# Kernel optimization log

Hardware: AMD Instinct MI355X
Metric: run time of the kernel (lower is better)

The kernel has to match this reference:

```python
import jax, jax.numpy as jnp
import numpy as np


def setup_inputs() -> dict:
    key = jax.random.key(0)
    k1, k2, k3, k4 = jax.random.split(key, 4)
    B, S, E, D = 8, 2048, 1024, 64
    return {
        "sequence": jax.random.normal(k1, (B, S, E), dtype=jnp.float32),
        "Wk": jax.random.normal(k2, (E, D), dtype=jnp.float32) * (E ** -0.5),
        "Wq": jax.random.normal(k3, (E, D), dtype=jnp.float32) * (E ** -0.5),
        "Wv": jax.random.normal(k4, (E, D), dtype=jnp.float32) * (E ** -0.5),
    }


def reference(sequence, Wk, Wq, Wv):
    # sequence: [B, S, E]; Wk/Wq/Wv: [E, D]
    B, S, E = sequence.shape
    D = Wk.shape[-1]
    k = sequence @ Wk  # [B, S, D]
    q = sequence @ Wq  # [B, S, D]
    v = sequence @ Wv  # [B, S, D]
    scores = jnp.einsum("bqd,bkd->bqk", q, k) * (D ** -0.5)  # [B, S, S]
    causal = jnp.tril(jnp.ones((S, S), dtype=bool))
    scores = jnp.where(causal, scores, -jnp.inf)
    attn = jax.nn.softmax(scores, axis=-1)  # [B, S, S]
    out = jnp.einsum("bqk,bkd->bqd", attn, v)  # [B, S, D]
    return (out, attn)
```

## Files before the change

kernel.cpp:

```cpp
#include <hip/hip_runtime.h>
#include <hip/hip_bf16.h>


typedef __attribute__((ext_vector_type(8))) __bf16 bf16x8;
typedef __attribute__((ext_vector_type(4))) float f32x4;

constexpr int S_LEN = 2048;

__device__ inline unsigned short f2bf(float f) {
  union { float f; unsigned u; } v; v.f = f;
  unsigned u = v.u + 0x7FFFu + ((v.u >> 16) & 1u);
  return (unsigned short)(u >> 16);
}
__device__ inline float bf2f(unsigned short s) {
  union { unsigned u; float f; } v; v.u = ((unsigned)s) << 16;
  return v.f;
}

__device__ inline uint4 pack8u(float4 f0, float4 f1) {
  union { __hip_bfloat162 h[4]; uint4 v; } u;
  u.h[0] = __float22bfloat162_rn(float2{f0.x, f0.y});
  u.h[1] = __float22bfloat162_rn(float2{f0.z, f0.w});
  u.h[2] = __float22bfloat162_rn(float2{f1.x, f1.y});
  u.h[3] = __float22bfloat162_rn(float2{f1.z, f1.w});
  return u.v;
}

__global__ __launch_bounds__(256) void wt_conv(
    const float* __restrict__ Wq, const float* __restrict__ Wk,
    const float* __restrict__ Wv, unsigned short* __restrict__ wt) {
  __shared__ float T[64][65];
  const int mat = blockIdx.y;
  const int k0 = blockIdx.x * 64;
  const float* W = (mat == 0) ? Wq : ((mat == 1) ? Wk : Wv);
  const int t = threadIdx.x;

  for (int s = 0; s < 4; ++s) {
    int rr = (t >> 4) + s * 16;
    int cc = (t & 15) * 4;
    float4 f = *(const float4*)(W + (size_t)(k0 + rr) * 64 + cc);
    T[rr][cc] = f.x; T[rr][cc + 1] = f.y; T[rr][cc + 2] = f.z; T[rr][cc + 3] = f.w;
  }
  __syncthreads();
  const float sc = (mat == 0) ? 0.125f : 1.0f;
  const int n = t >> 2, kc = (t & 3) * 16;
  union { unsigned short s[16]; uint4 v[2]; } tmp;
  for (int i = 0; i < 16; ++i) tmp.s[i] = f2bf(T[kc + i][n] * sc);
  unsigned short* dst = wt + (size_t)(mat * 64 + n) * 1024 + k0 + kc;
  *(uint4*)dst = tmp.v[0];
  *(uint4*)(dst + 8) = tmp.v[1];
}

__global__ __launch_bounds__(256) void qkv_gemm(
    const float* __restrict__ seq, const unsigned short* __restrict__ wt,
    unsigned short* __restrict__ qb, unsigned short* __restrict__ kb,
    unsigned short* __restrict__ vt) {
  __shared__ unsigned short As[2][32][72];
  const int row0 = blockIdx.x * 32;
  const int t = threadIdx.x;
  const int wv = t >> 6, lane = t & 63, lm = lane & 15, lq = lane >> 4;

  f32x4 acc[6];
  for (int i = 0; i < 6; ++i) acc[i] = (f32x4){0.f, 0.f, 0.f, 0.f};

  const int srow = t >> 3, skc = (t & 7) * 8;
  const float* ap = seq + (size_t)(row0 + srow) * 1024 + skc;

  float4 f0 = *(const float4*)ap;
  float4 f1 = *(const float4*)(ap + 4);
  *(uint4*)&As[0][srow][skc] = pack8u(f0, f1);

  for (int i = 0; i < 16; ++i) {
    if (i < 15) {
      f0 = *(const float4*)(ap + (i + 1) * 64);
      f1 = *(const float4*)(ap + (i + 1) * 64 + 4);
    }
    __syncthreads();
    const int buf = i & 1;
    for (int ks = 0; ks < 2; ++ks) {
      bf16x8 a0 = *(const bf16x8*)&As[buf][lm][ks * 32 + lq * 8];
      bf16x8 a1 = *(const bf16x8*)&As[buf][16 + lm][ks * 32 + lq * 8];
      for (int nt = 0; nt < 3; ++nt) {
        const unsigned short* bp =
            wt + (size_t)(wv * 48 + nt * 16 + lm) * 1024 + i * 64 + ks * 32 + lq * 8;
        bf16x8 bfr = *(const bf16x8*)bp;
        acc[nt] = __builtin_amdgcn_mfma_f32_16x16x32_bf16(a0, bfr, acc[nt], 0, 0, 0);
        acc[3 + nt] = __builtin_amdgcn_mfma_f32_16x16x32_bf16(a1, bfr, acc[3 + nt], 0, 0, 0);
      }
    }
    if (i < 15) *(uint4*)&As[buf ^ 1][srow][skc] = pack8u(f0, f1);
  }

  const int bb = row0 >> 11;
  const int s0 = row0 & (S_LEN - 1);
  for (int nt = 0; nt < 3; ++nt) {
    int ng = wv * 48 + nt * 16 + lm;
    int mat = ng >> 6, d = ng & 63;
    for (int mt = 0; mt < 2; ++mt) {
      f32x4 v = acc[mt * 3 + nt];
      if (mat == 2) {
        ushort4 u;
        u.x = f2bf(v[0]); u.y = f2bf(v[1]); u.z = f2bf(v[2]); u.w = f2bf(v[3]);
        *(ushort4*)(vt + ((size_t)(bb * 64 + d)) * S_LEN + s0 + mt * 16 + lq * 4) = u;
      } else {
        unsigned short* dst = mat ? kb : qb;
        for (int r = 0; r < 4; ++r)
          dst[(size_t)(row0 + mt * 16 + lq * 4 + r) * 64 + d] = f2bf(v[r]);
      }
    }
  }
}

__global__ __launch_bounds__(256) void attn_stats(
    const unsigned short* __restrict__ qb, const unsigned short* __restrict__ kb,
    float* __restrict__ lbuf) {
  __shared__ unsigned short Ks[128][72];
  const int q0 = blockIdx.x * 64, c0 = blockIdx.y * 512, b = blockIdx.z;
  if (c0 >= q0 + 64) return;
  const int kend = min(c0 + 512, q0 + 64);
  const int t = threadIdx.x, wv = t >> 6, lane = t & 63, lm = lane & 15, lq = lane >> 4;

  const unsigned short* qp = qb + ((size_t)(b * S_LEN + q0 + wv * 16 + lm)) * 64 + lq * 8;
  bf16x8 qf0 = *(const bf16x8*)qp;
  bf16x8 qf1 = *(const bf16x8*)(qp + 32);
  const int rw0 = q0 + wv * 16;

  float lp[4] = {0.f, 0.f, 0.f, 0.f};
  const int sr = t >> 3, sc = (t & 7) * 8;

  for (int kk = c0; kk < kend; kk += 128) {
    __syncthreads();
    const unsigned short* src = kb + ((size_t)(b * S_LEN + kk)) * 64;
    for (int j = 0; j < 4; ++j)
      *(uint4*)&Ks[j * 32 + sr][sc] = *(const uint4*)(src + (size_t)(j * 32 + sr) * 64 + sc);
    __syncthreads();
    if (kk <= rw0 + 15) {
      int ktmax = min(8, (rw0 + 15 - kk) / 16 + 1);
      for (int kt = 0; kt < ktmax; ++kt) {
        int key = kk + kt * 16 + lm;
        f32x4 z = (f32x4){0.f, 0.f, 0.f, 0.f};
        bf16x8 k0 = *(const bf16x8*)&Ks[kt * 16 + lm][lq * 8];
        bf16x8 k1 = *(const bf16x8*)&Ks[kt * 16 + lm][32 + lq * 8];
        z = __builtin_amdgcn_mfma_f32_16x16x32_bf16(qf0, k0, z, 0, 0, 0);
        z = __builtin_amdgcn_mfma_f32_16x16x32_bf16(qf1, k1, z, 0, 0, 0);
        for (int r = 0; r < 4; ++r) {
          float e = __expf(z[r]);
          lp[r] += (key <= rw0 + lq * 4 + r) ? e : 0.f;
        }
      }
    }
  }
  for (int off = 1; off < 16; off <<= 1)
    for (int r = 0; r < 4; ++r) lp[r] += __shfl_xor(lp[r], off);
  if (lm == 0)
    for (int r = 0; r < 4; ++r)
      unsafeAtomicAdd(&lbuf[b * S_LEN + rw0 + lq * 4 + r], lp[r]);
}

__global__ __launch_bounds__(256) void attn_write(
    const unsigned short* __restrict__ qb, const unsigned short* __restrict__ kb,
    const unsigned short* __restrict__ vt, const float* __restrict__ lbuf,
    float* __restrict__ outp, float* __restrict__ attnp) {
  __shared__ unsigned short Ks[256][72];
  __shared__ unsigned short Ps[4][16][72];
  const int q0 = blockIdx.x * 64, c0 = blockIdx.y * 256, b = blockIdx.z;
  const int t = threadIdx.x, wv = t >> 6, lane = t & 63, lm = lane & 15, lq = lane >> 4;
  float* arow = attnp + (size_t)b * S_LEN * S_LEN;

  if (c0 >= q0 + 64) {
    const int col = (t & 63) * 4, r0 = t >> 6;
    float4 z4 = {0.f, 0.f, 0.f, 0.f};
    for (int rr = r0; rr < 64; rr += 4)
      *(float4*)(arow + (size_t)(q0 + rr) * S_LEN + c0 + col) = z4;
    return;
  }

  {
    const int sr = t >> 3, sc = (t & 7) * 8;
    const unsigned short* src = kb + ((size_t)(b * S_LEN + c0)) * 64;
    for (int j = 0; j < 8; ++j)
      *(uint4*)&Ks[j * 32 + sr][sc] = *(const uint4*)(src + (size_t)(j * 32 + sr) * 64 + sc);
  }
  const unsigned short* qp = qb + ((size_t)(b * S_LEN + q0 + wv * 16 + lm)) * 64 + lq * 8;
  bf16x8 qf0 = *(const bf16x8*)qp;
  bf16x8 qf1 = *(const bf16x8*)(qp + 32);
  const int rw0 = q0 + wv * 16;

  float il[4];
  for (int r = 0; r < 4; ++r) il[r] = 1.0f / lbuf[b * S_LEN + rw0 + lq * 4 + r];

  f32x4 o[4];
  for (int i = 0; i < 4; ++i) o[i] = (f32x4){0.f, 0.f, 0.f, 0.f};
  __syncthreads();

  for (int st = 0; st < 4; ++st) {
    const int kk0 = c0 + st * 64;
    if (kk0 > rw0 + 15) {
      float4 z4 = {0.f, 0.f, 0.f, 0.f};
      for (int r4 = 0; r4 < 4; ++r4)
        *(float4*)(arow + (size_t)(rw0 + r4 * 4 + lq) * S_LEN + kk0 + lm * 4) = z4;
      continue;
    }
    f32x4 c4[4];
    for (int kt = 0; kt < 4; ++kt) {
      f32x4 z = (f32x4){0.f, 0.f, 0.f, 0.f};
      bf16x8 k0 = *(const bf16x8*)&Ks[st * 64 + kt * 16 + lm][lq * 8];
      bf16x8 k1 = *(const bf16x8*)&Ks[st * 64 + kt * 16 + lm][32 + lq * 8];
      z = __builtin_amdgcn_mfma_f32_16x16x32_bf16(qf0, k0, z, 0, 0, 0);
      z = __builtin_amdgcn_mfma_f32_16x16x32_bf16(qf1, k1, z, 0, 0, 0);
      c4[kt] = z;
    }
    bf16x8 vf[2][4];
    for (int ks2 = 0; ks2 < 2; ++ks2)
      for (int nt = 0; nt < 4; ++nt)
        vf[ks2][nt] = *(const bf16x8*)(vt + ((size_t)(b * 64 + nt * 16 + lm)) * S_LEN +
                                       kk0 + ks2 * 32 + lq * 8);
    for (int kt = 0; kt < 4; ++kt) {
      int key = kk0 + kt * 16 + lm;
      for (int r = 0; r < 4; ++r) {
        int rw = rw0 + lq * 4 + r;
        float p = (key > rw) ? 0.f : __expf(c4[kt][r]) * il[r];
        Ps[wv][lq * 4 + r][kt * 16 + lm] = f2bf(p);
      }
    }
    for (int ks2 = 0; ks2 < 2; ++ks2) {
      bf16x8 pa = *(const bf16x8*)&Ps[wv][lm][ks2 * 32 + lq * 8];
      for (int nt = 0; nt < 4; ++nt)
        o[nt] = __builtin_amdgcn_mfma_f32_16x16x32_bf16(pa, vf[ks2][nt], o[nt], 0, 0, 0);
    }
    for (int r4 = 0; r4 < 4; ++r4) {
      int row2 = r4 * 4 + lq;
      ushort4 u = *(const ushort4*)&Ps[wv][row2][lm * 4];
      float4 f;
      f.x = bf2f(u.x); f.y = bf2f(u.y); f.z = bf2f(u.z); f.w = bf2f(u.w);
      *(float4*)(arow + (size_t)(rw0 + row2) * S_LEN + kk0 + lm * 4) = f;
    }
  }

  for (int nt = 0; nt < 4; ++nt)
    for (int r = 0; r < 4; ++r)
      unsafeAtomicAdd(outp + ((size_t)(b * S_LEN + rw0 + lq * 4 + r)) * 64 + nt * 16 + lm,
                      o[nt][r]);
}

extern "C" void kernel_launch(void* const* d_in, const int* in_sizes, int n_in,
                              void* d_out, int out_size, void* d_ws, size_t ws_size,
                              hipStream_t stream) {
  const float* seq = (const float*)d_in[0];
  const float* Wk  = (const float*)d_in[1];
  const float* Wq  = (const float*)d_in[2];
  const float* Wv  = (const float*)d_in[3];

  float* outp = (float*)d_out;
  float* attnp = outp + (size_t)8 * S_LEN * 64;

  unsigned short* qb = (unsigned short*)d_ws;
  unsigned short* kb = qb + (size_t)16384 * 64;
  unsigned short* vt = kb + (size_t)16384 * 64;
  unsigned short* wt = vt + (size_t)8 * 64 * S_LEN;
  float* lbuf = (float*)(wt + (size_t)192 * 1024);

  hipMemsetAsync(lbuf, 0, (size_t)16384 * 4, stream);
  hipMemsetAsync(outp, 0, (size_t)8 * S_LEN * 64 * 4, stream);

  wt_conv<<<dim3(16, 3), 256, 0, stream>>>(Wq, Wk, Wv, wt);
  qkv_gemm<<<dim3(512, 1), 256, 0, stream>>>(seq, wt, qb, kb, vt);
  attn_stats<<<dim3(32, 4, 8), 256, 0, stream>>>(qb, kb, lbuf);
  attn_write<<<dim3(32, 8, 8), 256, 0, stream>>>(qb, kb, vt, lbuf, outp, attnp);
}
```

Before: 250.9 us.

## Stage weights in LDS for QKV GEMM, drop K LDS staging, use nontemporal attn stores

The QKV GEMM now runs with 512 threads and double-buffers both the activation tile and the full 192-column weight tile in shared memory, so B fragments are no longer fetched from global memory by every wave. The attention stats and write kernels drop their shared-memory K staging and the syncthreads around it, reading K fragments straight from global/L2 with unrolled loops. The large fp32 attention-matrix writes, including the zero fill above the diagonal, switch to nontemporal stores to avoid polluting the cache. Together these aim to cut global re-reads and cache pressure from the roughly 134 MB attention output, at the cost of more LDS per GEMM block and uncoalesced direct K loads.

```diff
diff --git a/kernel.cpp b/kernel.cpp
--- a/kernel.cpp
+++ b/kernel.cpp
@@ -17,13 +17,8 @@
   return v.f;
 }
 
-__device__ inline uint4 pack8u(float4 f0, float4 f1) {
-  union { __hip_bfloat162 h[4]; uint4 v; } u;
-  u.h[0] = __float22bfloat162_rn(float2{f0.x, f0.y});
-  u.h[1] = __float22bfloat162_rn(float2{f0.z, f0.w});
-  u.h[2] = __float22bfloat162_rn(float2{f1.x, f1.y});
-  u.h[3] = __float22bfloat162_rn(float2{f1.z, f1.w});
-  return u.v;
+__device__ inline void nt_store4(float* p, f32x4 v) {
+  __builtin_nontemporal_store(v, (f32x4*)p);
 }
 
 __global__ __launch_bounds__(256) void wt_conv(
@@ -51,62 +46,83 @@
   *(uint4*)(dst + 8) = tmp.v[1];
 }
 
-__global__ __launch_bounds__(256) void qkv_gemm(
+__global__ __launch_bounds__(512, 4) void qkv_gemm(
     const float* __restrict__ seq, const unsigned short* __restrict__ wt,
     unsigned short* __restrict__ qb, unsigned short* __restrict__ kb,
     unsigned short* __restrict__ vt) {
   __shared__ unsigned short As[2][32][72];
+  __shared__ unsigned short Bs[2][192][72];
   const int row0 = blockIdx.x * 32;
   const int t = threadIdx.x;
   const int wv = t >> 6, lane = t & 63, lm = lane & 15, lq = lane >> 4;
-
-  f32x4 acc[6];
-  for (int i = 0; i < 6; ++i) acc[i] = (f32x4){0.f, 0.f, 0.f, 0.f};
-
-  const int srow = t >> 3, skc = (t & 7) * 8;
+  const int wm = wv >> 2, wn = wv & 3;
+
+  f32x4 acc[3];
+  for (int i = 0; i < 3; ++i) acc[i] = (f32x4){0.f, 0.f, 0.f, 0.f};
+
+  const int srow = t >> 4, skc = (t & 15) * 4;
   const float* ap = seq + (size_t)(row0 + srow) * 1024 + skc;
 
-  float4 f0 = *(const float4*)ap;
-  float4 f1 = *(const float4*)(ap + 4);
-  *(uint4*)&As[0][srow][skc] = pack8u(f0, f1);
+  float4 fa = *(const float4*)ap;
+  uint4 bseg[3];
+  for (int it = 0; it < 3; ++it) {
+    int seg = t + it * 512, n = seg >> 3, kc = (seg & 7) * 8;
+    bseg[it] = *(const uint4*)(wt + (size_t)n * 1024 + kc);
+  }
+  {
+    union { __hip_bfloat162 h[2]; uint2 v; } u;
+    u.h[0] = __float22bfloat162_rn(float2{fa.x, fa.y});
+    u.h[1] = __float22bfloat162_rn(float2{fa.z, fa.w});
+    *(uint2*)&As[0][srow][skc] = u.v;
+    for (int it = 0; it < 3; ++it) {
+      int seg = t + it * 512, n = seg >> 3, kc = (seg & 7) * 8;
+      *(uint4*)&Bs[0][n][kc] = bseg[it];
+    }
+  }
 
   for (int i = 0; i < 16; ++i) {
     if (i < 15) {
-      f0 = *(const float4*)(ap + (i + 1) * 64);
-      f1 = *(const float4*)(ap + (i + 1) * 64 + 4);
+      fa = *(const float4*)(ap + (i + 1) * 64);
+      for (int it = 0; it < 3; ++it) {
+        int seg = t + it * 512, n = seg >> 3, kc = (seg & 7) * 8;
+        bseg[it] = *(const uint4*)(wt + (size_t)n * 1024 + (i + 1) * 64 + kc);
+      }
     }
     __syncthreads();
     const int buf = i & 1;
     for (int ks = 0; ks < 2; ++ks) {
-      bf16x8 a0 = *(const bf16x8*)&As[buf][lm][ks * 32 + lq * 8];
-      bf16x8 a1 = *(const bf16x8*)&As[buf][16 + lm][ks * 32 + lq * 8];
+      bf16x8 af = *(const bf16x8*)&As[buf][wm * 16 + lm][ks * 32 + lq * 8];
       for (int nt = 0; nt < 3; ++nt) {
-        const unsigned short* bp =
-            wt + (size_t)(wv * 48 + nt * 16 + lm) * 1024 + i * 64 + ks * 32 + lq * 8;
-        bf16x8 bfr = *(const bf16x8*)bp;
-        acc[nt] = __builtin_amdgcn_mfma_f32_16x16x32_bf16(a0, bfr, acc[nt], 0, 0, 0);
-        acc[3 + nt] = __builtin_amdgcn_mfma_f32_16x16x32_bf16(a1, bfr, acc[3 + nt], 0, 0, 0);
-      }
-    }
-    if (i < 15) *(uint4*)&As[buf ^ 1][srow][skc] = pack8u(f0, f1);
+        bf16x8 bfr = *(const bf16x8*)&Bs[buf][wn * 48 + nt * 16 + lm][ks * 32 + lq * 8];
+        acc[nt] = __builtin_amdgcn_mfma_f32_16x16x32_bf16(af, bfr, acc[nt], 0, 0, 0);
+      }
+    }
+    if (i < 15) {
+      union { __hip_bfloat162 h[2]; uint2 v; } u;
+      u.h[0] = __float22bfloat162_rn(float2{fa.x, fa.y});
+      u.h[1] = __float22bfloat162_rn(float2{fa.z, fa.w});
+      *(uint2*)&As[buf ^ 1][srow][skc] = u.v;
+      for (int it = 0; it < 3; ++it) {
+        int seg = t + it * 512, n = seg >> 3, kc = (seg & 7) * 8;
+        *(uint4*)&Bs[buf ^ 1][n][kc] = bseg[it];
+      }
+    }
   }
 
   const int bb = row0 >> 11;
   const int s0 = row0 & (S_LEN - 1);
   for (int nt = 0; nt < 3; ++nt) {
-    int ng = wv * 48 + nt * 16 + lm;
+    int ng = wn * 48 + nt * 16 + lm;
     int mat = ng >> 6, d = ng & 63;
-    for (int mt = 0; mt < 2; ++mt) {
-      f32x4 v = acc[mt * 3 + nt];
-      if (mat == 2) {
-        ushort4 u;
-        u.x = f2bf(v[0]); u.y = f2bf(v[1]); u.z = f2bf(v[2]); u.w = f2bf(v[3]);
-        *(ushort4*)(vt + ((size_t)(bb * 64 + d)) * S_LEN + s0 + mt * 16 + lq * 4) = u;
-      } else {
-        unsigned short* dst = mat ? kb : qb;
-        for (int r = 0; r < 4; ++r)
-          dst[(size_t)(row0 + mt * 16 + lq * 4 + r) * 64 + d] = f2bf(v[r]);
-      }
+    f32x4 v = acc[nt];
+    if (mat == 2) {
+      ushort4 u;
+      u.x = f2bf(v[0]); u.y = f2bf(v[1]); u.z = f2bf(v[2]); u.w = f2bf(v[3]);
+      *(ushort4*)(vt + ((size_t)(bb * 64 + d)) * S_LEN + s0 + wm * 16 + lq * 4) = u;
+    } else {
+      unsigned short* dst = mat ? kb : qb;
+      for (int r = 0; r < 4; ++r)
+        dst[(size_t)(row0 + wm * 16 + lq * 4 + r) * 64 + d] = f2bf(v[r]);
     }
   }
 }
@@ -114,40 +130,31 @@
 __global__ __launch_bounds__(256) void attn_stats(
     const unsigned short* __restrict__ qb, const unsigned short* __restrict__ kb,
     float* __restrict__ lbuf) {
-  __shared__ unsigned short Ks[128][72];
   const int q0 = blockIdx.x * 64, c0 = blockIdx.y * 512, b = blockIdx.z;
   if (c0 >= q0 + 64) return;
-  const int kend = min(c0 + 512, q0 + 64);
   const int t = threadIdx.x, wv = t >> 6, lane = t & 63, lm = lane & 15, lq = lane >> 4;
-
-  const unsigned short* qp = qb + ((size_t)(b * S_LEN + q0 + wv * 16 + lm)) * 64 + lq * 8;
+  const int rw0 = q0 + wv * 16;
+
+  const unsigned short* qp = qb + ((size_t)(b * S_LEN + rw0 + lm)) * 64 + lq * 8;
   bf16x8 qf0 = *(const bf16x8*)qp;
   bf16x8 qf1 = *(const bf16x8*)(qp + 32);
-  const int rw0 = q0 + wv * 16;
 
   float lp[4] = {0.f, 0.f, 0.f, 0.f};
-  const int sr = t >> 3, sc = (t & 7) * 8;
-
-  for (int kk = c0; kk < kend; kk += 128) {
-    __syncthreads();
-    const unsigned short* src = kb + ((size_t)(b * S_LEN + kk)) * 64;
-    for (int j = 0; j < 4; ++j)
-      *(uint4*)&Ks[j * 32 + sr][sc] = *(const uint4*)(src + (size_t)(j * 32 + sr) * 64 + sc);
-    __syncthreads();
-    if (kk <= rw0 + 15) {
-      int ktmax = min(8, (rw0 + 15 - kk) / 16 + 1);
-      for (int kt = 0; kt < ktmax; ++kt) {
-        int key = kk + kt * 16 + lm;
-        f32x4 z = (f32x4){0.f, 0.f, 0.f, 0.f};
-        bf16x8 k0 = *(const bf16x8*)&Ks[kt * 16 + lm][lq * 8];
-        bf16x8 k1 = *(const bf16x8*)&Ks[kt * 16 + lm][32 + lq * 8];
-        z = __builtin_amdgcn_mfma_f32_16x16x32_bf16(qf0, k0, z, 0, 0, 0);
-        z = __builtin_amdgcn_mfma_f32_16x16x32_bf16(qf1, k1, z, 0, 0, 0);
-        for (int r = 0; r < 4; ++r) {
-          float e = __expf(z[r]);
-          lp[r] += (key <= rw0 + lq * 4 + r) ? e : 0.f;
-        }
-      }
+  const unsigned short* kbase = kb + ((size_t)b * S_LEN) * 64;
+  const int kend = min(c0 + 512, rw0 + 16);
+
+#pragma unroll 4
+  for (int key0 = c0; key0 < kend; key0 += 16) {
+    const unsigned short* kp = kbase + (size_t)(key0 + lm) * 64 + lq * 8;
+    bf16x8 k0 = *(const bf16x8*)kp;
+    bf16x8 k1 = *(const bf16x8*)(kp + 32);
+    f32x4 z = (f32x4){0.f, 0.f, 0.f, 0.f};
+    z = __builtin_amdgcn_mfma_f32_16x16x32_bf16(qf0, k0, z, 0, 0, 0);
+    z = __builtin_amdgcn_mfma_f32_16x16x32_bf16(qf1, k1, z, 0, 0, 0);
+    const int key = key0 + lm;
+    for (int r = 0; r < 4; ++r) {
+      float e = __expf(z[r]);
+      lp[r] += (key <= rw0 + lq * 4 + r) ? e : 0.f;
     }
   }
   for (int off = 1; off < 16; off <<= 1)
@@ -161,7 +168,6 @@
     const unsigned short* __restrict__ qb, const unsigned short* __restrict__ kb,
     const unsigned short* __restrict__ vt, const float* __restrict__ lbuf,
     float* __restrict__ outp, float* __restrict__ attnp) {
-  __shared__ unsigned short Ks[256][72];
   __shared__ unsigned short Ps[4][16][72];
   const int q0 = blockIdx.x * 64, c0 = blockIdx.y * 256, b = blockIdx.z;
   const int t = threadIdx.x, wv = t >> 6, lane = t & 63, lm = lane & 15, lq = lane >> 4;
@@ -169,43 +175,39 @@
 
   if (c0 >= q0 + 64) {
     const int col = (t & 63) * 4, r0 = t >> 6;
-    float4 z4 = {0.f, 0.f, 0.f, 0.f};
+    f32x4 z4 = (f32x4){0.f, 0.f, 0.f, 0.f};
     for (int rr = r0; rr < 64; rr += 4)
-      *(float4*)(arow + (size_t)(q0 + rr) * S_LEN + c0 + col) = z4;
+      nt_store4(arow + (size_t)(q0 + rr) * S_LEN + c0 + col, z4);
     return;
   }
 
-  {
-    const int sr = t >> 3, sc = (t & 7) * 8;
-    const unsigned short* src = kb + ((size_t)(b * S_LEN + c0)) * 64;
-    for (int j = 0; j < 8; ++j)
-      *(uint4*)&Ks[j * 32 + sr][sc] = *(const uint4*)(src + (size_t)(j * 32 + sr) * 64 + sc);
-  }
   const unsigned short* qp = qb + ((size_t)(b * S_LEN + q0 + wv * 16 + lm)) * 64 + lq * 8;
   bf16x8 qf0 = *(const bf16x8*)qp;
   bf16x8 qf1 = *(const bf16x8*)(qp + 32);
   const int rw0 = q0 + wv * 16;
+  const unsigned short* kbase = kb + ((size_t)b * S_LEN) * 64;
 
   float il[4];
   for (int r = 0; r < 4; ++r) il[r] = 1.0f / lbuf[b * S_LEN + rw0 + lq * 4 + r];
 
   f32x4 o[4];
   for (int i = 0; i < 4; ++i) o[i] = (f32x4){0.f, 0.f, 0.f, 0.f};
-  __syncthreads();
 
   for (int st = 0; st < 4; ++st) {
     const int kk0 = c0 + st * 64;
     if (kk0 > rw0 + 15) {
-      float4 z4 = {0.f, 0.f, 0.f, 0.f};
+      f32x4 z4 = (f32x4){0.f, 0.f, 0.f, 0.f};
       for (int r4 = 0; r4 < 4; ++r4)
-        *(float4*)(arow + (size_t)(rw0 + r4 * 4 + lq) * S_LEN + kk0 + lm * 4) = z4;
+        nt_store4(arow + (size_t)(rw0 + r4 * 4 + lq) * S_LEN + kk0 + lm * 4, z4);
       continue;
     }
     f32x4 c4[4];
+#pragma unroll
     for (int kt = 0; kt < 4; ++kt) {
+      const unsigned short* kp = kbase + (size_t)(kk0 + kt * 16 + lm) * 64 + lq * 8;
+      bf16x8 k0 = *(const bf16x8*)kp;
+      bf16x8 k1 = *(const bf16x8*)(kp + 32);
       f32x4 z = (f32x4){0.f, 0.f, 0.f, 0.f};
-      bf16x8 k0 = *(const bf16x8*)&Ks[st * 64 + kt * 16 + lm][lq * 8];
-      bf16x8 k1 = *(const bf16x8*)&Ks[st * 64 + kt * 16 + lm][32 + lq * 8];
       z = __builtin_amdgcn_mfma_f32_16x16x32_bf16(qf0, k0, z, 0, 0, 0);
       z = __builtin_amdgcn_mfma_f32_16x16x32_bf16(qf1, k1, z, 0, 0, 0);
       c4[kt] = z;
@@ -231,9 +233,9 @@
     for (int r4 = 0; r4 < 4; ++r4) {
       int row2 = r4 * 4 + lq;
       ushort4 u = *(const ushort4*)&Ps[wv][row2][lm * 4];
-      float4 f;
-      f.x = bf2f(u.x); f.y = bf2f(u.y); f.z = bf2f(u.z); f.w = bf2f(u.w);
-      *(float4*)(arow + (size_t)(rw0 + row2) * S_LEN + kk0 + lm * 4) = f;
+      f32x4 f;
+      f[0] = bf2f(u.x); f[1] = bf2f(u.y); f[2] = bf2f(u.z); f[3] = bf2f(u.w);
+      nt_store4(arow + (size_t)(rw0 + row2) * S_LEN + kk0 + lm * 4, f);
     }
   }
 
@@ -264,7 +266,7 @@
   hipMemsetAsync(outp, 0, (size_t)8 * S_LEN * 64 * 4, stream);
 
   wt_conv<<<dim3(16, 3), 256, 0, stream>>>(Wq, Wk, Wv, wt);
-  qkv_gemm<<<dim3(512, 1), 256, 0, stream>>>(seq, wt, qb, kb, vt);
+  qkv_gemm<<<dim3(512, 1), 512, 0, stream>>>(seq, wt, qb, kb, vt);
   attn_stats<<<dim3(32, 4, 8), 256, 0, stream>>>(qb, kb, lbuf);
   attn_write<<<dim3(32, 8, 8), 256, 0, stream>>>(qb, kb, vt, lbuf, outp, attnp);
 }
```

New measurement: 322.1 us. 28.4% more time.
